# Kernel optimization log

Hardware: AMD Instinct MI355X
Metric: run time of the kernel (lower is better)

The kernel has to match this reference:

```python
import jax, jax.numpy as jnp
import numpy as np

HID, NH, HD = 1024, 16, 64
B, S = 2, 2048


def _gammas(nh):
    # gammas = 1 - exp(linspace(log(1/512), log(1/32), nh))
    lin = np.linspace(np.log(1.0 / 512.0), np.log(1.0 / 32.0), nh)
    return jnp.asarray(1.0 - np.exp(lin), dtype=jnp.float32)


def setup_inputs() -> dict:
    key = jax.random.key(0)
    ks = jax.random.split(key, 6)
    x = jax.random.normal(ks[0], (B, S, HID), dtype=jnp.float32)
    # Per-head retention projection weights (Retention has its own q/k/v of [head_size, head_size])
    wq = jax.random.normal(ks[1], (NH, HD, HD), dtype=jnp.float32) / HD
    wk = jax.random.normal(ks[2], (NH, HD, HD), dtype=jnp.float32) / HD
    wv = jax.random.normal(ks[3], (NH, HD, HD), dtype=jnp.float32) / HD
    w1 = jax.random.normal(ks[4], (HID, HID), dtype=jnp.float32) / HID
    w2 = jax.random.normal(ks[5], (HID, HID), dtype=jnp.float32) / HID
    gn_scale = jnp.ones((HID,), dtype=jnp.float32)
    gn_bias = jnp.zeros((HID,), dtype=jnp.float32)
    return {"x": x, "wq": wq, "wk": wk, "wv": wv, "w1": w1, "w2": w2,
            "gn_scale": gn_scale, "gn_bias": gn_bias}


def reference(x, wq, wk, wv, w1, w2, gn_scale, gn_bias):
    b, s, h = x.shape
    nh, hd = wq.shape[0], wq.shape[1]
    gammas = _gammas(nh)  # [nh]

    xh = x.reshape(b, s, nh, hd)
    q = jnp.einsum('bsnd,nde->bsne', xh, wq)
    k = jnp.einsum('bsnd,nde->bsne', xh, wk)
    v = jnp.einsum('bsnd,nde->bsne', xh, wv)

    # causal decay mask D[n, s, t] = gamma_n ** (s - t) for s >= t else 0
    idx = jnp.arange(s)
    diff = (idx[:, None] - idx[None, :]).astype(jnp.float32)  # [s, s]
    safe = jnp.maximum(diff, 0.0)
    D = jnp.where(diff >= 0,
                  jnp.exp(safe[None] * jnp.log(gammas)[:, None, None]),
                  0.0)  # [nh, s, s]

    scores = jnp.einsum('bsnd,btnd->bnst', q, k) * D[None]      # [b, nh, s, s]
    ret = jnp.einsum('bnst,btnd->bsnd', scores, v)              # [b, s, nh, hd]

    # GroupNorm(num_groups=nh, num_channels=h) over flattened [b*s, h]:
    # normalize within each head-group of hd channels, affine per-channel, eps=1e-5
    mean = ret.mean(axis=-1, keepdims=True)
    var = ret.var(axis=-1, keepdims=True)
    norm = (ret - mean) / jnp.sqrt(var + 1e-5)
    norm = norm.reshape(b, s, h) * gn_scale + gn_bias

    gate = jnp.matmul(x, w1)
    out = gate * jax.nn.sigmoid(gate) + norm  # swish-gated branch + retention
    return jnp.matmul(out, w2)
```

## Files before the change

### kernel.cpp

```cpp
#include <hip/hip_runtime.h>

#define HIDD 1024
#define NHH  16
#define HDD  64
#define BBB  2
#define SSS  2048
#define BS   (BBB * SSS)

typedef __attribute__((ext_vector_type(8))) _Float16 half8;
typedef __attribute__((ext_vector_type(4))) _Float16 half4;
typedef __attribute__((ext_vector_type(2))) __fp16   fp16x2;
typedef __attribute__((ext_vector_type(4))) float    f32x4;

#define LSCALE 2048.0f
#define LINV   (1.0f / 2048.0f)

static __device__ __forceinline__ f32x4 mfma16h(half8 a, half8 b, f32x4 c) {
    return __builtin_amdgcn_mfma_f32_16x16x32_f16(a, b, c, 0, 0, 0);
}

static __device__ __forceinline__ void split2h(float v, _Float16& h, _Float16& l) {
    h = (_Float16)v;
    l = (_Float16)((v - (float)h) * LSCALE);
}

static __device__ __forceinline__ void gl_lds16(const _Float16* g, _Float16* l) {
    __builtin_amdgcn_global_load_lds(
        (const __attribute__((address_space(1))) unsigned int*)g,
        (__attribute__((address_space(3))) unsigned int*)l,
        16, 0, 0);
}

__global__ __launch_bounds__(256) void k_wprep(const float* __restrict__ wq,
                                               const float* __restrict__ wk,
                                               const float* __restrict__ wv,
                                               _Float16* __restrict__ WTh,
                                               _Float16* __restrict__ WTl) {
    const int blk = blockIdx.x;
    const int mat = blk >> 4, n = blk & 15;
    const float* src = (mat == 0 ? wq : mat == 1 ? wk : wv) + (size_t)n * 4096;
    for (int c = threadIdx.x; c < 4096; c += 256) {
        int e = c >> 6, d = c & 63;
        float v = src[d * 64 + e];
        _Float16 h, l;
        split2h(v, h, l);
        WTh[(size_t)blk * 4096 + c] = h;
        WTl[(size_t)blk * 4096 + c] = l;
    }
}

__global__ __launch_bounds__(512) void k_proj_mfma(const float* __restrict__ x,
                                                   const _Float16* __restrict__ WTh,
                                                   const _Float16* __restrict__ WTl,
                                                   _Float16* __restrict__ Qh, _Float16* __restrict__ Ql,
                                                   _Float16* __restrict__ Kh, _Float16* __restrict__ Kl,
                                                   _Float16* __restrict__ VTh, _Float16* __restrict__ VTl) {
    const int n  = blockIdx.y;
    const int R0 = blockIdx.x * 128;
    const int tid = threadIdx.x;
    const int w = tid >> 6, lane = tid & 63;
    const int hi = lane >> 4, lo = lane & 15;

    __shared__ __align__(16) _Float16 smem[27648];

    half8 ah[2], al[2];
#pragma unroll
    for (int kf = 0; kf < 2; kf++) {
        const float* xp = x + (size_t)(R0 + 16 * w + lo) * HIDD + n * HDD + kf * 32 + 8 * hi;
        float4 v0 = *(const float4*)xp;
        float4 v1 = *(const float4*)(xp + 4);
        float vv[8] = { v0.x, v0.y, v0.z, v0.w, v1.x, v1.y, v1.z, v1.w };
#pragma unroll
        for (int j = 0; j < 8; ++j) {
            _Float16 h, l;
            split2h(vv[j], h, l);
            ah[kf][j] = h; al[kf][j] = l;
        }
    }

    for (int c = tid; c < 3072; c += 512) {
        int m = c >> 10, rest = c & 1023, hl = rest >> 9, cc = rest & 511;
        int r = cc >> 3, j8 = (cc & 7) << 3;
        const _Float16* src = (hl ? WTl : WTh) + ((size_t)(m * NHH + n)) * 4096 + r * 64 + j8;
        *(half8*)&smem[(m * 2 + hl) * 4608 + r * 72 + j8] = *(const half8*)src;
    }
    __syncthreads();

    const int bq = R0 >> 11;
    const int sr = R0 & 2047;
    const size_t bn = (size_t)(bq * NHH + n);
    float vkeep[4][4][2];

    for (int mat = 0; mat < 3; ++mat) {
        const _Float16* bh_base = smem + (mat * 2 + 0) * 4608;
        const _Float16* bl_base = smem + (mat * 2 + 1) * 4608;
        f32x4 a0[4], a1[4];
#pragma unroll
        for (int eb = 0; eb < 4; ++eb) {
            a0[eb] = (f32x4){0.f, 0.f, 0.f, 0.f};
            a1[eb] = (f32x4){0.f, 0.f, 0.f, 0.f};
        }
#pragma unroll
        for (int eb = 0; eb < 4; ++eb) {
            half8 bh0 = *(const half8*)&bh_base[(16 * eb + lo) * 72 + 8 * hi];
            half8 bh1 = *(const half8*)&bh_base[(16 * eb + lo) * 72 + 32 + 8 * hi];
            half8 bl0 = *(const half8*)&bl_base[(16 * eb + lo) * 72 + 8 * hi];
            half8 bl1 = *(const half8*)&bl_base[(16 * eb + lo) * 72 + 32 + 8 * hi];
            a0[eb] = mfma16h(ah[0], bh0, a0[eb]);
            a0[eb] = mfma16h(ah[1], bh1, a0[eb]);
            a1[eb] = mfma16h(ah[0], bl0, a1[eb]);
            a1[eb] = mfma16h(al[0], bh0, a1[eb]);
            a1[eb] = mfma16h(ah[1], bl1, a1[eb]);
            a1[eb] = mfma16h(al[1], bh1, a1[eb]);
        }

        if (mat < 2) {
            _Float16* Dh = (mat == 0) ? Qh : Kh;
            _Float16* Dl = (mat == 0) ? Ql : Kl;
#pragma unroll
            for (int eb = 0; eb < 4; ++eb)
#pragma unroll
                for (int r = 0; r < 4; ++r) {
                    int gr = R0 + 16 * w + 4 * hi + r;
                    int s = gr & 2047;
                    float val = a0[eb][r] + a1[eb][r] * LINV;
                    _Float16 h, l;
                    split2h(val, h, l);
                    size_t idx = (bn * SSS + s) * HDD + 16 * eb + lo;
                    Dh[idx] = h; Dl[idx] = l;
                }
        } else {
#pragma unroll
            for (int eb = 0; eb < 4; ++eb)
#pragma unroll
                for (int r = 0; r < 4; ++r) {
                    vkeep[eb][r][0] = a0[eb][r];
                    vkeep[eb][r][1] = a1[eb][r];
                }
        }
    }

    __syncthreads();
    _Float16* tbh = smem;
    _Float16* tbl = smem + 8704;
#pragma unroll
    for (int eb = 0; eb < 4; ++eb)
#pragma unroll
        for (int r = 0; r < 4; ++r) {
            int rl = 16 * w + 4 * hi + r;
            int ch = 16 * eb + lo;
            _Float16 h, l;
            split2h(vkeep[eb][r][0] + vkeep[eb][r][1] * LINV, h, l);
            tbh[ch * 136 + rl] = h;
            tbl[ch * 136 + rl] = l;
        }
    __syncthreads();
    for (int c = tid; c < 1024; c += 512) {
        int ch = c >> 4, s8 = (c & 15) << 3;
        int a64 = s8 & 64;
        int s0 = s8 & 63;
        int basePerm = a64 + (s0 & 32) + ((s0 >> 3) & 3) * 4;
        const _Float16* th = &tbh[ch * 136];
        const _Float16* tl = &tbl[ch * 136];
        half4 h0 = *(const half4*)(th + basePerm);
        half4 h1 = *(const half4*)(th + basePerm + 16);
        half4 l0 = *(const half4*)(tl + basePerm);
        half4 l1 = *(const half4*)(tl + basePerm + 16);
        half8 oh = {h0[0], h0[1], h0[2], h0[3], h1[0], h1[1], h1[2], h1[3]};
        half8 ol = {l0[0], l0[1], l0[2], l0[3], l1[0], l1[1], l1[2], l1[3]};
        size_t gi = (bn * HDD + ch) * SSS + sr + s8;
        *(half8*)(VTh + gi) = oh;
        *(half8*)(VTl + gi) = ol;
    }
}

__global__ __launch_bounds__(256) void k_ret_mfma(const _Float16* __restrict__ Qh, const _Float16* __restrict__ Ql,
                                                  const _Float16* __restrict__ Kh, const _Float16* __restrict__ Kl,
                                                  const _Float16* __restrict__ VTh, const _Float16* __restrict__ VTl,
                                                  const float* __restrict__ gns,
                                                  const float* __restrict__ gnb,
                                                  float* __restrict__ normb,
                                                  unsigned* __restrict__ counter) {
    const int tid = threadIdx.x;
    const int w = tid >> 6, lane = tid & 63;
    const int hi = lane >> 4, lo = lane & 15;

    __shared__ __align__(16) _Float16 ksh[4096];
    __shared__ __align__(16) _Float16 ksl[4096];
    __shared__ __align__(16) _Float16 vsh[4096];
    __shared__ __align__(16) _Float16 vsl[4096];
    __shared__ unsigned sitem;

    const int ks0 = ((hi ^ (lo & 7)) << 3);
    const int ks1 = (((4 + hi) ^ (lo & 7)) << 3);
    const int vs0 = ((hi ^ ((lo >> 1) & 3)) << 3);
    size_t goffK = (size_t)(lane >> 3) * HDD + (size_t)((((lane & 7) ^ ((lane >> 3) & 7))) << 3);
    size_t goffV = (size_t)(lane >> 2) * SSS + (size_t)((((lane & 3) ^ ((lane >> 3) & 3))) << 3);

    const double l512 = -6.2383246250395075;
    const double l32  = -3.4657359027997265;

    while (true) {
        if (tid == 0) sitem = atomicAdd(counter, 1u);
        __syncthreads();
        const unsigned it = sitem;
        __syncthreads();
        if (it >= 1024u) break;

        const int qt = 31 - (int)(it >> 5);
        const int n  = (int)(it & 15);
        const int b  = (int)((it >> 4) & 1);

        double lin = l512 + (double)n * (l32 - l512) / 15.0;
        float gamma = (float)(1.0 - exp(lin));
        float l2g = log2f(gamma);
        int dmax = (int)(16.0f / (-l2g)) + 1;

        const int qb = qt * 64;
        const int qw = qb + 16 * w;
        int stb_start = (qb > dmax) ? ((qb - dmax) >> 5) : 0;
        const int stb_end  = 2 * qt + 1;
        const int stb_diag = qw >> 5;

        const size_t bn = (size_t)(b * NHH + n);
        const _Float16* Qhp = Qh + bn * SSS * HDD;
        const _Float16* Qlp = Ql + bn * SSS * HDD;
        const _Float16* Khp = Kh + bn * SSS * HDD;
        const _Float16* Klp = Kl + bn * SSS * HDD;
        const _Float16* Vhp = VTh + bn * HDD * SSS;
        const _Float16* Vlp = VTl + bn * HDD * SSS;

        half8 qfh[2], qfl[2];
#pragma unroll
        for (int kf = 0; kf < 2; kf++) {
            size_t o = (size_t)(qw + lo) * HDD + kf * 32 + 8 * hi;
            qfh[kf] = *(const half8*)(Qhp + o);
            qfl[kf] = *(const half8*)(Qlp + o);
        }

        f32x4 acc0[4], acc1[4];
#pragma unroll
        for (int e = 0; e < 4; e++) {
            acc0[e] = (f32x4){0.f, 0.f, 0.f, 0.f};
            acc1[e] = (f32x4){0.f, 0.f, 0.f, 0.f};
        }

        const _Float16* sg = (w == 0) ? Khp : (w == 1) ? Klp : (w == 2) ? Vhp : Vlp;
        _Float16* slds = (w == 0) ? ksh : (w == 1) ? ksl : (w == 2) ? vsh : vsl;
        const size_t goff = (w < 2) ? goffK : goffV;

        auto issue = [&](int tbase, int pbuf) {
            _Float16* Lb = slds + pbuf * 2048;
            if (w < 2) {
#pragma unroll
                for (int i = 0; i < 4; ++i)
                    gl_lds16(sg + (size_t)(tbase + 8 * i) * HDD + goff, Lb + i * 512);
            } else {
#pragma unroll
                for (int i = 0; i < 4; ++i)
                    gl_lds16(sg + (size_t)(16 * i) * SSS + tbase + goff, Lb + i * 512);
            }
        };

        float ftile = exp2f((float)(qw + lo - stb_start * 32) * l2g);
        const float gi16   = exp2f(-16.0f * l2g);
        const float ginv32 = exp2f(-32.0f * l2g);
        float f4[4];
#pragma unroll
        for (int r = 0; r < 4; ++r) f4[r] = exp2f(-(float)(4 * hi + r) * l2g);

        int pb = 0;
        issue(stb_start * 32, 0);
        __syncthreads();

        for (int stb = stb_start; stb <= stb_end; ++stb) {
            const int tbase = stb * 32;
            if (stb < stb_end) issue(tbase + 32, pb ^ 1);

            const bool active = (tbase <= qw + 15) && (tbase + 31 >= qw - dmax);
            if (active) {
                const bool dm = (stb == stb_diag);
                const _Float16* kh_ = &ksh[pb * 2048];
                const _Float16* kl_ = &ksl[pb * 2048];
                const _Float16* vh_ = &vsh[pb * 2048];
                const _Float16* vl_ = &vsl[pb * 2048];
                _Float16 phv[2][4], plv[2][4];
#pragma unroll
                for (int tt = 0; tt < 2; ++tt) {
                    int rb = (16 * tt + lo) * 64;
                    half8 kh0 = *(const half8*)&kh_[rb + ks0];
                    half8 kh1 = *(const half8*)&kh_[rb + ks1];
                    half8 kl0 = *(const half8*)&kl_[rb + ks0];
                    half8 kl1 = *(const half8*)&kl_[rb + ks1];
                    f32x4 s0 = (f32x4){0.f, 0.f, 0.f, 0.f};
                    f32x4 s1 = (f32x4){0.f, 0.f, 0.f, 0.f};
                    s0 = mfma16h(kh0, qfh[0], s0);
                    s0 = mfma16h(kh1, qfh[1], s0);
                    s1 = mfma16h(kl0, qfh[0], s1);
                    s1 = mfma16h(kh0, qfl[0], s1);
                    s1 = mfma16h(kl1, qfh[1], s1);
                    s1 = mfma16h(kh1, qfl[1], s1);
                    const float g = tt ? ftile * gi16 : ftile;
                    float pv[4];
#pragma unroll
                    for (int r = 0; r < 4; r++) {
                        float p = (s0[r] + s1[r] * LINV) * (g * f4[r]);
                        if (dm) {
                            int diff = (qw + lo) - (tbase + 16 * tt + 4 * hi + r);
                            if (diff < 0) p = 0.0f;
                        }
                        pv[r] = p;
                    }
                    fp16x2 h01 = __builtin_amdgcn_cvt_pkrtz(pv[0], pv[1]);
                    fp16x2 h23 = __builtin_amdgcn_cvt_pkrtz(pv[2], pv[3]);
                    fp16x2 l01 = __builtin_amdgcn_cvt_pkrtz((pv[0] - (float)h01[0]) * LSCALE,
                                                            (pv[1] - (float)h01[1]) * LSCALE);
                    fp16x2 l23 = __builtin_amdgcn_cvt_pkrtz((pv[2] - (float)h23[0]) * LSCALE,
                                                            (pv[3] - (float)h23[1]) * LSCALE);
                    phv[tt][0] = (_Float16)h01[0]; phv[tt][1] = (_Float16)h01[1];
                    phv[tt][2] = (_Float16)h23[0]; phv[tt][3] = (_Float16)h23[1];
                    plv[tt][0] = (_Float16)l01[0]; plv[tt][1] = (_Float16)l01[1];
                    plv[tt][2] = (_Float16)l23[0]; plv[tt][3] = (_Float16)l23[1];
                }
                half8 pfh = (half8){phv[0][0], phv[0][1], phv[0][2], phv[0][3],
                                    phv[1][0], phv[1][1], phv[1][2], phv[1][3]};
                half8 pfl = (half8){plv[0][0], plv[0][1], plv[0][2], plv[0][3],
                                    plv[1][0], plv[1][1], plv[1][2], plv[1][3]};
#pragma unroll
                for (int e = 0; e < 4; e++) {
                    int vb = (16 * e + lo) * 32 + vs0;
                    half8 vh0 = *(const half8*)&vh_[vb];
                    half8 vl0 = *(const half8*)&vl_[vb];
                    acc0[e] = mfma16h(pfh, vh0, acc0[e]);
                    acc1[e] = mfma16h(pfh, vl0, acc1[e]);
                    acc1[e] = mfma16h(pfl, vh0, acc1[e]);
                }
            }
            ftile *= ginv32;
            __syncthreads();
            pb ^= 1;
        }

        f32x4 accf[4];
#pragma unroll
        for (int e = 0; e < 4; e++)
#pragma unroll
            for (int r = 0; r < 4; r++)
                accf[e][r] = acc0[e][r] + acc1[e][r] * LINV;

        float s[4], sq[4];
#pragma unroll
        for (int r = 0; r < 4; r++) {
            s[r] = 0.f; sq[r] = 0.f;
#pragma unroll
            for (int e = 0; e < 4; e++) { float v = accf[e][r]; s[r] += v; sq[r] += v * v; }
        }
#pragma unroll
        for (int mask = 1; mask < 16; mask <<= 1)
#pragma unroll
            for (int r = 0; r < 4; r++) {
                s[r]  += __shfl_xor(s[r],  mask);
                sq[r] += __shfl_xor(sq[r], mask);
            }
#pragma unroll
        for (int e = 0; e < 4; e++)
#pragma unroll
            for (int r = 0; r < 4; r++) {
                float mean = s[r] * (1.0f / 64.0f);
                float var  = sq[r] * (1.0f / 64.0f) - mean * mean;
                float rstd = rsqrtf(var + 1e-5f);
                int ch = 16 * e + lo;
                int sg2 = qw + 4 * hi + r;
                float nv = (accf[e][r] - mean) * rstd;
                nv = nv * gns[n * 64 + ch] + gnb[n * 64 + ch];
                normb[((size_t)b * SSS + sg2) * HIDD + n * 64 + ch] = nv;
            }
        __syncthreads();
    }
}

__global__ __launch_bounds__(256) void k_prep3(const float* __restrict__ x,
                                               const float* __restrict__ w1,
                                               const float* __restrict__ w2,
                                               _Float16* __restrict__ xh,
                                               _Float16* __restrict__ w1t,
                                               _Float16* __restrict__ w2t) {
    const int z = blockIdx.z;
    if (z == 0) {
        size_t base = (((size_t)blockIdx.y * 32 + blockIdx.x) * 256 + threadIdx.x) * 16;
#pragma unroll
        for (int j = 0; j < 4; ++j) {
            float4 v = *(const float4*)(x + base + 4 * j);
            half4 o = { (_Float16)v.x, (_Float16)v.y, (_Float16)v.z, (_Float16)v.w };
            *(half4*)(xh + base + 4 * j) = o;
        }
    } else {
        const float* src = (z == 1) ? w1 : w2;
        _Float16* dst = (z == 1) ? w1t : w2t;
        __shared__ float ls[32][33];
        int kb = blockIdx.y * 32, nb = blockIdx.x * 32;
        int tx = threadIdx.x & 31, ty = threadIdx.x >> 5;
#pragma unroll
        for (int i = 0; i < 4; i++) {
            int r = ty + 8 * i;
            ls[r][tx] = src[(size_t)(kb + r) * HIDD + nb + tx];
        }
        __syncthreads();
#pragma unroll
        for (int i = 0; i < 4; i++) {
            int r = ty + 8 * i;
            dst[(size_t)(nb + r) * HIDD + kb + tx] = (_Float16)ls[tx][r];
        }
    }
}

template <int MODE>
__global__ __launch_bounds__(256) void k_gemm_h(const _Float16* __restrict__ A,
                                                const _Float16* __restrict__ Bt,
                                                const float* __restrict__ normb,
                                                _Float16* __restrict__ Y,
                                                float* __restrict__ Out) {
    const int Rb = blockIdx.x * 128, Cb = blockIdx.y * 128;
    const int tid = threadIdx.x, w = tid >> 6, lane = tid & 63;
    const int hi = lane >> 4, lo = lane & 15;
    const int wm = w >> 1, wn = w & 1;

    __shared__ __align__(16) _Float16 as[2][128 * 64];
    __shared__ __align__(16) _Float16 bs[2][128 * 64];

    f32x4 acc[4][4];
#pragma unroll
    for (int m = 0; m < 4; m++)
#pragma unroll
        for (int nn = 0; nn < 4; nn++) acc[m][nn] = (f32x4){0.f, 0.f, 0.f, 0.f};

    const _Float16* gM = (w < 2) ? (A + (size_t)(Rb + 64 * (w & 1)) * HIDD)
                                 : (Bt + (size_t)(Cb + 64 * (w & 1)) * HIDD);
    const int wsel = (w < 2) ? 0 : 1;
    const size_t gofs = (size_t)(lane >> 3) * HIDD
                      + (size_t)((((lane & 7) ^ ((lane >> 3) & 7))) << 3);

    auto issue = [&](int kk, int pbuf) {
        _Float16* gL = (wsel ? bs[pbuf] : as[pbuf]) + (w & 1) * 64 * 64;
#pragma unroll
        for (int i = 0; i < 8; ++i)
            gl_lds16(gM + (size_t)(8 * i) * HIDD + kk * 64 + gofs, gL + i * 512);
    };

    int rsw[2];
#pragma unroll
    for (int kf = 0; kf < 2; kf++) rsw[kf] = ((4 * kf + hi) ^ (lo & 7)) << 3;

    int pb = 0;
    issue(0, 0);
    __syncthreads();

    for (int kk = 0; kk < 16; ++kk) {
        if (kk < 15) issue(kk + 1, pb ^ 1);

        half8 af[4][2], bf[4][2];
#pragma unroll
        for (int m = 0; m < 4; m++) {
            int row = 64 * wm + 16 * m + lo;
#pragma unroll
            for (int kf = 0; kf < 2; kf++)
                af[m][kf] = *(const half8*)&as[pb][row * 64 + rsw[kf]];
        }
#pragma unroll
        for (int nn = 0; nn < 4; nn++) {
            int row = 64 * wn + 16 * nn + lo;
#pragma unroll
            for (int kf = 0; kf < 2; kf++)
                bf[nn][kf] = *(const half8*)&bs[pb][row * 64 + rsw[kf]];
        }
#pragma unroll
        for (int m = 0; m < 4; m++)
#pragma unroll
            for (int nn = 0; nn < 4; nn++) {
                acc[m][nn] = mfma16h(af[m][0], bf[nn][0], acc[m][nn]);
                acc[m][nn] = mfma16h(af[m][1], bf[nn][1], acc[m][nn]);
            }
        __syncthreads();
        pb ^= 1;
    }

#pragma unroll
    for (int m = 0; m < 4; m++)
#pragma unroll
        for (int nn = 0; nn < 4; nn++)
#pragma unroll
            for (int r = 0; r < 4; r++) {
                int row = Rb + 64 * wm + 16 * m + 4 * hi + r;
                int col = Cb + 64 * wn + 16 * nn + lo;
                float v = acc[m][nn][r];
                size_t idx = (size_t)row * HIDD + col;
                if (MODE == 0) {
                    float sw = v / (1.0f + expf(-v));
                    float y = sw + normb[idx];
                    Y[idx] = (_Float16)y;
                } else {
                    Out[idx] = v;
                }
            }
}

extern "C" void kernel_launch(void* const* d_in, const int* in_sizes, int n_in,
                              void* d_out, int out_size, void* d_ws, size_t ws_size,
                              hipStream_t stream) {
    const float* x   = (const float*)d_in[0];
    const float* wq  = (const float*)d_in[1];
    const float* wk  = (const float*)d_in[2];
    const float* wv  = (const float*)d_in[3];
    const float* w1  = (const float*)d_in[4];
    const float* w2  = (const float*)d_in[5];
    const float* gns = (const float*)d_in[6];
    const float* gnb = (const float*)d_in[7];
    float* out = (float*)d_out;

    char* base = (char*)d_ws;
    size_t off = 0;
    auto carve = [&](size_t bytes) -> void* {
        void* p = base + off;
        off += (bytes + 255) & ~(size_t)255;
        return p;
    };
    _Float16* Qh  = (_Float16*)carve((size_t)BS * HIDD * 2);
    _Float16* Ql  = (_Float16*)carve((size_t)BS * HIDD * 2);
    _Float16* Kh  = (_Float16*)carve((size_t)BS * HIDD * 2);
    _Float16* Kl  = (_Float16*)carve((size_t)BS * HIDD * 2);
    _Float16* VTh = (_Float16*)carve((size_t)BS * HIDD * 2);
    _Float16* VTl = (_Float16*)carve((size_t)BS * HIDD * 2);
    float*    normb = (float*)carve((size_t)BS * HIDD * 4);
    _Float16* WTh = (_Float16*)normb;
    _Float16* WTl = WTh + (size_t)48 * 4096;
    _Float16* xh  = Qh;
    _Float16* w1t = Kh;
    _Float16* w2t = Kh + (size_t)HIDD * HIDD;
    _Float16* yh  = VTh;
    unsigned* counter = (unsigned*)d_out;
    (void)ws_size; (void)in_sizes; (void)n_in; (void)out_size;

    k_wprep<<<48, 256, 0, stream>>>(wq, wk, wv, WTh, WTl);
    k_proj_mfma<<<dim3(BS / 128, NHH), 512, 0, stream>>>(x, WTh, WTl,
                                                         Qh, Ql, Kh, Kl, VTh, VTl);
    (void)hipMemsetAsync(counter, 0, sizeof(unsigned), stream);
    k_ret_mfma<<<512, 256, 0, stream>>>(Qh, Ql, Kh, Kl, VTh, VTl,
                                        gns, gnb, normb, counter);
    k_prep3<<<dim3(32, 32, 3), 256, 0, stream>>>(x, w1, w2, xh, w1t, w2t);
    k_gemm_h<0><<<dim3(BS / 128, HIDD / 128), 256, 0, stream>>>(xh, w1t, normb, yh, nullptr);
    k_gemm_h<1><<<dim3(BS / 128, HIDD / 128), 256, 0, stream>>>(yh, w2t, nullptr, nullptr, out);
}
```

Baseline: 143.7 us.

## Quad-buffer K/V LDS tiles and process two tiles per barrier

```diff
diff --git a/kernel.cpp b/kernel.cpp
--- a/kernel.cpp
+++ b/kernel.cpp
@@ -185,10 +185,10 @@
     const int w = tid >> 6, lane = tid & 63;
     const int hi = lane >> 4, lo = lane & 15;
 
-    __shared__ __align__(16) _Float16 ksh[4096];
-    __shared__ __align__(16) _Float16 ksl[4096];
-    __shared__ __align__(16) _Float16 vsh[4096];
-    __shared__ __align__(16) _Float16 vsl[4096];
+    __shared__ __align__(16) _Float16 ksh[8192];
+    __shared__ __align__(16) _Float16 ksl[8192];
+    __shared__ __align__(16) _Float16 vsh[8192];
+    __shared__ __align__(16) _Float16 vsl[8192];
     __shared__ unsigned sitem;
 
     const int ks0 = ((hi ^ (lo & 7)) << 3);
@@ -245,20 +245,23 @@
             acc1[e] = (f32x4){0.f, 0.f, 0.f, 0.f};
         }
 
-        const _Float16* sg = (w == 0) ? Khp : (w == 1) ? Klp : (w == 2) ? Vhp : Vlp;
+        const _Float16* sg = (w == 0) ? (Khp + goffK) : (w == 1) ? (Klp + goffK)
+                           : (w == 2) ? (Vhp + goffV) : (Vlp + goffV);
         _Float16* slds = (w == 0) ? ksh : (w == 1) ? ksl : (w == 2) ? vsh : vsl;
-        const size_t goff = (w < 2) ? goffK : goffV;
+        const bool isK = (w < 2);
 
         auto issue = [&](int tbase, int pbuf) {
             _Float16* Lb = slds + pbuf * 2048;
-            if (w < 2) {
+            if (isK) {
+                const _Float16* gp = sg + (size_t)tbase * HDD;
 #pragma unroll
                 for (int i = 0; i < 4; ++i)
-                    gl_lds16(sg + (size_t)(tbase + 8 * i) * HDD + goff, Lb + i * 512);
+                    gl_lds16(gp + (size_t)(8 * i) * HDD, Lb + i * 512);
             } else {
+                const _Float16* gp = sg + tbase;
 #pragma unroll
                 for (int i = 0; i < 4; ++i)
-                    gl_lds16(sg + (size_t)(16 * i) * SSS + tbase + goff, Lb + i * 512);
+                    gl_lds16(gp + (size_t)(16 * i) * SSS, Lb + i * 512);
             }
         };
 
@@ -269,21 +272,15 @@
 #pragma unroll
         for (int r = 0; r < 4; ++r) f4[r] = exp2f(-(float)(4 * hi + r) * l2g);
 
-        int pb = 0;
-        issue(stb_start * 32, 0);
-        __syncthreads();
-
-        for (int stb = stb_start; stb <= stb_end; ++stb) {
+        auto work = [&](int stb, int bi) {
             const int tbase = stb * 32;
-            if (stb < stb_end) issue(tbase + 32, pb ^ 1);
-
             const bool active = (tbase <= qw + 15) && (tbase + 31 >= qw - dmax);
             if (active) {
                 const bool dm = (stb == stb_diag);
-                const _Float16* kh_ = &ksh[pb * 2048];
-                const _Float16* kl_ = &ksl[pb * 2048];
-                const _Float16* vh_ = &vsh[pb * 2048];
-                const _Float16* vl_ = &vsl[pb * 2048];
+                const _Float16* kh_ = &ksh[bi * 2048];
+                const _Float16* kl_ = &ksl[bi * 2048];
+                const _Float16* vh_ = &vsh[bi * 2048];
+                const _Float16* vl_ = &vsl[bi * 2048];
                 _Float16 phv[2][4], plv[2][4];
 #pragma unroll
                 for (int tt = 0; tt < 2; ++tt) {
@@ -337,8 +334,20 @@
                 }
             }
             ftile *= ginv32;
+        };
+
+        issue(stb_start * 32, 0);
+        if (stb_start + 1 <= stb_end) issue(stb_start * 32 + 32, 1);
+        __syncthreads();
+
+        for (int stb = stb_start; stb <= stb_end; stb += 2) {
+            const int bi = (stb - stb_start) & 3;
+            if (stb + 2 <= stb_end) issue((stb + 2) * 32, (bi + 2) & 3);
+            if (stb + 3 <= stb_end) issue((stb + 3) * 32, (bi + 3) & 3);
+
+            work(stb, bi);
+            if (stb + 1 <= stb_end) work(stb + 1, (bi + 1) & 3);
             __syncthreads();
-            pb ^= 1;
         }
 
         f32x4 accf[4];
```

Measured after the change: 135.5 us (median of 2 runs). -5.7%, faster.
